# Performance work log

Measured on AMD Instinct MI355X. Metric: run time of the kernel, lower is better.

The kernel has to match this reference:

```python
import jax, jax.numpy as jnp
import numpy as np

EMBED_DIM = 1024
NUM_HEADS = 16
HEAD_DIM = EMBED_DIM // NUM_HEADS


def setup_inputs() -> dict:
    key = jax.random.key(0)
    k_x, k_wqkv, k_bqkv, k_wo, k_bo = jax.random.split(key, 5)
    B, T, C = 4, 2048, EMBED_DIM
    bound = 1.0 / np.sqrt(C)
    return {
        "x": jax.random.normal(k_x, (B, T, C), dtype=jnp.float32),
        "w_qkv": jax.random.uniform(k_wqkv, (C, 3 * C), jnp.float32, -bound, bound),
        "b_qkv": jax.random.uniform(k_bqkv, (3 * C,), jnp.float32, -bound, bound),
        "w_out": jax.random.uniform(k_wo, (C, C), jnp.float32, -bound, bound),
        "b_out": jax.random.uniform(k_bo, (C,), jnp.float32, -bound, bound),
    }


def reference(x, w_qkv, b_qkv, w_out, b_out):
    B, T, C = x.shape
    H, D = NUM_HEADS, HEAD_DIM
    qkv = x @ w_qkv + b_qkv                       # [B,T,3C]
    qkv = qkv.reshape(B, T, 3, H, D)
    q, k, v = qkv[:, :, 0], qkv[:, :, 1], qkv[:, :, 2]  # [B,T,H,D]
    scale = 1.0 / np.sqrt(D).astype(np.float32)
    scores = jnp.einsum("bqhd,bkhd->bhqk", q, k) * scale  # [B,H,T,T]
    causal = jnp.tril(jnp.ones((T, T), dtype=bool))
    scores = jnp.where(causal, scores, -jnp.inf)
    attn = jax.nn.softmax(scores, axis=-1)
    # dropout p=0.0 / eval mode -> identity
    ctx = jnp.einsum("bhqk,bkhd->bqhd", attn, v).reshape(B, T, C)
    return ctx @ w_out + b_out
```

## Files before the change

kernel.cpp:

```cpp
#include <hip/hip_runtime.h>
#include <hip/hip_bf16.h>

#define NB 4
#define NT 2048
#define NC 1024
#define NH 16
#define ND 64
#define BT (NB*NT)
#define LOG2E 1.4426950408889634f
#define NEG_BIG (-3.0e38f)
#define MLC 28.853900817779268f

typedef __attribute__((ext_vector_type(8))) short bf16x8;
typedef __attribute__((ext_vector_type(4))) float f32x4;

static __device__ __forceinline__ short f2bf(float f) {
    union { float f; unsigned u; } v; v.f = f;
    unsigned r = (v.u + 0x7fffu + ((v.u >> 16) & 1u)) >> 16;
    return (short)r;
}

static __device__ __forceinline__ unsigned pk2(float a, float b) {
#if __has_builtin(__builtin_amdgcn_cvt_pk_bf16_f32)
    auto v = __builtin_amdgcn_cvt_pk_bf16_f32(a, b);
    union { decltype(v) v; unsigned u; } c; c.v = v; return c.u;
#else
    return (unsigned)(unsigned short)f2bf(a) | ((unsigned)(unsigned short)f2bf(b) << 16);
#endif
}

static __device__ __forceinline__ f32x4 mfma16(bf16x8 a, bf16x8 b, f32x4 c) {
    return __builtin_amdgcn_mfma_f32_16x16x32_bf16(a, b, c, 0, 0, 0);
}

static __device__ __forceinline__ float fexp2(float x) {
#if __has_builtin(__builtin_amdgcn_exp2f)
    return __builtin_amdgcn_exp2f(x);
#else
    return exp2f(x);
#endif
}

template<int GOFF>
static __device__ __forceinline__ void gload_lds16(const short* g, short* l) {
    __builtin_amdgcn_global_load_lds(
        (const __attribute__((address_space(1))) void*)g,
        (__attribute__((address_space(3))) void*)l,
        16, GOFF, 0);
}

static __device__ __forceinline__ void wait_all() {
    __builtin_amdgcn_s_waitcnt(0);
    __builtin_amdgcn_sched_barrier(0);
}
static __device__ __forceinline__ void wait_lgkm() {
    __builtin_amdgcn_s_waitcnt(0xc07f);
    __builtin_amdgcn_sched_barrier(0);
}

__global__ __launch_bounds__(256)
void xcvt(const float* __restrict__ x, short* __restrict__ xb)
{
    const size_t i = ((size_t)blockIdx.x * 256 + threadIdx.x) * 8;
    float4 f0 = *(const float4*)(x + i);
    float4 f1 = *(const float4*)(x + i + 4);
    uint4 p;
    p.x = pk2(f0.x, f0.y); p.y = pk2(f0.z, f0.w);
    p.z = pk2(f1.x, f1.y); p.w = pk2(f1.z, f1.w);
    *(uint4*)(xb + i) = p;
}

__global__ __launch_bounds__(256)
void transpose_w(const float* __restrict__ w, short* __restrict__ wt, int R, int Cn)
{
    __shared__ short t[64][72];
    const int tid = threadIdx.x;
    const int r0 = blockIdx.x * 64;
    const int c0 = blockIdx.y * 64;
    {
        const int rl = tid >> 2, c4 = (tid & 3) << 4;
        const float* src = w + (size_t)(r0 + rl) * Cn + c0 + c4;
        float4 f0 = *(const float4*)(src + 0);
        float4 f1 = *(const float4*)(src + 4);
        float4 f2 = *(const float4*)(src + 8);
        float4 f3 = *(const float4*)(src + 12);
        short* d = &t[rl][c4];
        d[0]=f2bf(f0.x); d[1]=f2bf(f0.y); d[2]=f2bf(f0.z); d[3]=f2bf(f0.w);
        d[4]=f2bf(f1.x); d[5]=f2bf(f1.y); d[6]=f2bf(f1.z); d[7]=f2bf(f1.w);
        d[8]=f2bf(f2.x); d[9]=f2bf(f2.y); d[10]=f2bf(f2.z); d[11]=f2bf(f2.w);
        d[12]=f2bf(f3.x); d[13]=f2bf(f3.y); d[14]=f2bf(f3.z); d[15]=f2bf(f3.w);
    }
    __syncthreads();
    {
        const int cl = tid >> 2, r4 = (tid & 3) << 4;
        bf16x8 p0, p1;
#pragma unroll
        for (int j = 0; j < 8; ++j) { p0[j] = t[r4 + j][cl]; p1[j] = t[r4 + 8 + j][cl]; }
        short* dst = wt + (size_t)(c0 + cl) * R + r0 + r4;
        *(bf16x8*)dst       = p0;
        *(bf16x8*)(dst + 8) = p1;
    }
}

__global__ __launch_bounds__(256)
void qkv_gemm(const short* __restrict__ xb, const short* __restrict__ wt,
              const float* __restrict__ bias,
              short* __restrict__ q, short* __restrict__ k, short* __restrict__ vt)
{
    __shared__ short aLds[128 * 64];
    __shared__ short bLds[128 * 64];
    const int tid  = threadIdx.x;
    const int lane = tid & 63;
    const int wave = tid >> 6;
    const int waveM = wave & 1;
    const int waveN = wave >> 1;
    const int quad = lane >> 4;
    const int l15  = lane & 15;
    const int l7   = l15 & 7;
    const int m0 = blockIdx.x * 128;
    const int n0 = blockIdx.y * 128;

    const int rsub   = lane >> 3;
    const int cchunk = (lane & 7) ^ rsub;
    const int gcol   = cchunk * 8;

    f32x4 acc[4][4];
#pragma unroll
    for (int i = 0; i < 4; ++i)
#pragma unroll
        for (int j = 0; j < 4; ++j) acc[i][j] = 0.0f;

    for (int k0 = 0; k0 < NC; k0 += 64) {
#pragma unroll
        for (int i = 0; i < 4; ++i) {
            const int rbase = wave * 32 + i * 8;
            gload_lds16<0>(xb + (size_t)(m0 + rbase + rsub) * NC + k0 + gcol,
                           &aLds[rbase * 64]);
        }
#pragma unroll
        for (int i = 0; i < 4; ++i) {
            const int rbase = wave * 32 + i * 8;
            gload_lds16<0>(wt + (size_t)(n0 + rbase + rsub) * NC + k0 + gcol,
                           &bLds[rbase * 64]);
        }
        __syncthreads();

#pragma unroll
        for (int kd = 0; kd < 2; ++kd) {
            bf16x8 af[4], bfr[4];
#pragma unroll
            for (int mi = 0; mi < 4; ++mi) {
                const int r = waveM*64 + mi*16 + l15;
                af[mi] = *(const bf16x8*)&aLds[r*64 + (((kd*4 + quad) ^ l7) * 8)];
            }
#pragma unroll
            for (int ni = 0; ni < 4; ++ni) {
                const int r = waveN*64 + ni*16 + l15;
                bfr[ni] = *(const bf16x8*)&bLds[r*64 + (((kd*4 + quad) ^ l7) * 8)];
            }
#pragma unroll
            for (int mi = 0; mi < 4; ++mi)
#pragma unroll
                for (int ni = 0; ni < 4; ++ni)
                    acc[mi][ni] = mfma16(af[mi], bfr[ni], acc[mi][ni]);
        }
        __syncthreads();
    }

#pragma unroll
    for (int mi = 0; mi < 4; ++mi) {
#pragma unroll
        for (int ni = 0; ni < 4; ++ni) {
            const int n = n0 + waveN*64 + ni*16 + l15;
            const float bb = bias[n];
            const int s = n >> 10;
            const int h = (n >> 6) & 15;
            const int d = n & 63;
#pragma unroll
            for (int r = 0; r < 4; ++r) {
                const int m = m0 + waveM*64 + mi*16 + quad*4 + r;
                const int b = m >> 11;
                const int t = m & (NT - 1);
                const float val = acc[mi][ni][r] + bb;
                const size_t bhx = (size_t)(b * NH + h);
                if (s == 0)      q [(bhx * NT + t) * ND + d] = f2bf(val * 0.125f);
                else if (s == 1) k [(bhx * NT + t) * ND + d] = f2bf(val);
                else             vt[(bhx * ND + d) * NT + t] = f2bf(val);
            }
        }
    }
}

__global__ __launch_bounds__(64)
void attn(const short* __restrict__ q, const short* __restrict__ k,
          const short* __restrict__ vt, short* __restrict__ ctx)
{
    __shared__ short kbuf[64 * 64];
    __shared__ short vbuf[64 * 64];
    __shared__ short pLds[32][72];
    const int lane = threadIdx.x;
    const int quad = lane >> 4;
    const int l15  = lane & 15;
    const int l7   = l15 & 7;
    const int bh = blockIdx.x;
    const int b  = bh >> 4;
    const int h  = bh & 15;

    const short* Qp = q  + (size_t)bh * NT * ND;
    const short* Kp = k  + (size_t)bh * NT * ND;
    const short* Vp = vt + (size_t)bh * ND * NT;

    const int srow   = lane >> 3;
    const int schunk = ((lane & 7) ^ srow) * 8;

    for (int half = 0; half < 2; ++half) {
        const int qtile = half ? (63 - (int)blockIdx.y) : (int)blockIdx.y;
        const int wq0 = qtile * 32;
        const int ktend = (wq0 + 95) >> 6;

        bf16x8 qf[2][2];
#pragma unroll
        for (int mi = 0; mi < 2; ++mi)
#pragma unroll
            for (int kd = 0; kd < 2; ++kd)
                qf[mi][kd] = *(const bf16x8*)(Qp + (size_t)(wq0 + mi*16 + l15) * ND + kd*32 + quad*8);

        f32x4 ot[4][2];
        f32x4 lv[2];
#pragma unroll
        for (int di = 0; di < 4; ++di)
#pragma unroll
            for (int mi = 0; mi < 2; ++mi) ot[di][mi] = 0.0f;
        lv[0] = 0.0f; lv[1] = 0.0f;

        const short* Kcur = Kp + srow * ND + schunk;
        const short* Vg[8];
#pragma unroll
        for (int g = 0; g < 8; ++g)
            Vg[g] = Vp + (size_t)(g*8 + srow) * NT + schunk;

#pragma unroll
        for (int g = 0; g < 8; ++g)
            gload_lds16<0>(Kcur + g * 512, &kbuf[g * 512]);
#pragma unroll
        for (int g = 0; g < 8; ++g)
            gload_lds16<0>(Vg[g], &vbuf[g * 512]);

        for (int kt = 0; kt < ktend; ++kt) {
            wait_all();

            bf16x8 kf[4][2], vf[4][2];
#pragma unroll
            for (int ni = 0; ni < 4; ++ni)
#pragma unroll
                for (int kd = 0; kd < 2; ++kd)
                    kf[ni][kd] = *(const bf16x8*)
                        &kbuf[(ni*16 + l15)*64 + (((kd*4 + quad) ^ l7) * 8)];
#pragma unroll
            for (int di = 0; di < 4; ++di)
#pragma unroll
                for (int kd = 0; kd < 2; ++kd)
                    vf[di][kd] = *(const bf16x8*)
                        &vbuf[(di*16 + l15)*64 + (((kd*4 + quad) ^ l7) * 8)];
            wait_lgkm();

            if (kt + 1 < ktend) {
                Kcur += 4096;
#pragma unroll
                for (int g = 0; g < 8; ++g)
                    gload_lds16<0>(Kcur + g * 512, &kbuf[g * 512]);
#pragma unroll
                for (int g = 0; g < 8; ++g) {
                    Vg[g] += 64;
                    gload_lds16<0>(Vg[g], &vbuf[g * 512]);
                }
            }

            const int kb = kt << 6;

            f32x4 st[4][2];
#pragma unroll
            for (int ni = 0; ni < 4; ++ni)
#pragma unroll
                for (int mi = 0; mi < 2; ++mi) {
                    st[ni][mi] = 0.0f;
                    st[ni][mi] = mfma16(kf[ni][0], qf[mi][0], st[ni][mi]);
                    st[ni][mi] = mfma16(kf[ni][1], qf[mi][1], st[ni][mi]);
                }

            if (kb + 63 > wq0) {
#pragma unroll
                for (int ni = 0; ni < 4; ++ni)
#pragma unroll
                    for (int mi = 0; mi < 2; ++mi) {
                        const int qrow = wq0 + mi*16 + l15;
#pragma unroll
                        for (int r = 0; r < 4; ++r) {
                            const int key = kb + ni*16 + quad*4 + r;
                            if (key > qrow) st[ni][mi][r] = NEG_BIG;
                        }
                    }
            }

#pragma unroll
            for (int mi = 0; mi < 2; ++mi) {
#pragma unroll
                for (int ni = 0; ni < 4; ++ni) {
#pragma unroll
                    for (int r = 0; r < 4; ++r)
                        st[ni][mi][r] = fexp2(fmaf(st[ni][mi][r], LOG2E, -MLC));
                    lv[mi] += st[ni][mi];
                    const f32x4 v = st[ni][mi];
                    *(uint2*)&pLds[mi*16 + l15][ni*16 + quad*4] =
                        make_uint2(pk2(v[0], v[1]), pk2(v[2], v[3]));
                }
            }

            bf16x8 pf[2][2];
#pragma unroll
            for (int mi = 0; mi < 2; ++mi)
#pragma unroll
                for (int kd = 0; kd < 2; ++kd)
                    pf[mi][kd] = *(const bf16x8*)&pLds[mi*16 + l15][kd*32 + quad*8];

#pragma unroll
            for (int di = 0; di < 4; ++di)
#pragma unroll
                for (int mi = 0; mi < 2; ++mi) {
                    ot[di][mi] = mfma16(vf[di][0], pf[mi][0], ot[di][mi]);
                    ot[di][mi] = mfma16(vf[di][1], pf[mi][1], ot[di][mi]);
                }
        }

#pragma unroll
        for (int mi = 0; mi < 2; ++mi) {
            float l = lv[mi][0] + lv[mi][1] + lv[mi][2] + lv[mi][3];
            l += __shfl_xor(l, 16);
            l += __shfl_xor(l, 32);
            const float inv = 1.0f / l;
            const int t = wq0 + mi*16 + l15;
            short* dst = ctx + ((size_t)(b * NT + t)) * NC + h*64 + quad*4;
#pragma unroll
            for (int di = 0; di < 4; ++di) {
                const f32x4 v = ot[di][mi] * inv;
                *(uint2*)(dst + di*16) = make_uint2(pk2(v[0], v[1]), pk2(v[2], v[3]));
            }
        }
        wait_all();
    }
}

__global__ __launch_bounds__(256)
void out_gemm(const short* __restrict__ a, const short* __restrict__ wt,
              const float* __restrict__ bias, float* __restrict__ out)
{
    __shared__ short aLds[128 * 64];
    __shared__ short bLds[128 * 64];
    const int tid  = threadIdx.x;
    const int lane = tid & 63;
    const int wave = tid >> 6;
    const int waveM = wave & 1;
    const int waveN = wave >> 1;
    const int quad = lane >> 4;
    const int l15  = lane & 15;
    const int l7   = l15 & 7;
    const int m0 = blockIdx.x * 128;
    const int n0 = blockIdx.y * 128;

    const int rsub   = lane >> 3;
    const int cchunk = (lane & 7) ^ rsub;
    const int gcol   = cchunk * 8;

    f32x4 acc[4][4];
#pragma unroll
    for (int i = 0; i < 4; ++i)
#pragma unroll
        for (int j = 0; j < 4; ++j) acc[i][j] = 0.0f;

    for (int k0 = 0; k0 < NC; k0 += 64) {
#pragma unroll
        for (int i = 0; i < 4; ++i) {
            const int rbase = wave * 32 + i * 8;
            gload_lds16<0>(a + (size_t)(m0 + rbase + rsub) * NC + k0 + gcol,
                           &aLds[rbase * 64]);
        }
#pragma unroll
        for (int i = 0; i < 4; ++i) {
            const int rbase = wave * 32 + i * 8;
            gload_lds16<0>(wt + (size_t)(n0 + rbase + rsub) * NC + k0 + gcol,
                           &bLds[rbase * 64]);
        }
        __syncthreads();

#pragma unroll
        for (int kd = 0; kd < 2; ++kd) {
            bf16x8 af[4], bfr[4];
#pragma unroll
            for (int mi = 0; mi < 4; ++mi) {
                const int r = waveM*64 + mi*16 + l15;
                af[mi] = *(const bf16x8*)&aLds[r*64 + (((kd*4 + quad) ^ l7) * 8)];
            }
#pragma unroll
            for (int ni = 0; ni < 4; ++ni) {
                const int r = waveN*64 + ni*16 + l15;
                bfr[ni] = *(const bf16x8*)&bLds[r*64 + (((kd*4 + quad) ^ l7) * 8)];
            }
#pragma unroll
            for (int mi = 0; mi < 4; ++mi)
#pragma unroll
                for (int ni = 0; ni < 4; ++ni)
                    acc[mi][ni] = mfma16(af[mi], bfr[ni], acc[mi][ni]);
        }
        __syncthreads();
    }

#pragma unroll
    for (int mi = 0; mi < 4; ++mi) {
#pragma unroll
        for (int ni = 0; ni < 4; ++ni) {
            const int n = n0 + waveN*64 + ni*16 + l15;
            const float bb = bias[n];
#pragma unroll
            for (int r = 0; r < 4; ++r) {
                const int m = m0 + waveM*64 + mi*16 + quad*4 + r;
                out[(size_t)m * NC + n] = acc[mi][ni][r] + bb;
            }
        }
    }
}

extern "C" void kernel_launch(void* const* d_in, const int* in_sizes, int n_in,
                              void* d_out, int out_size, void* d_ws, size_t ws_size,
                              hipStream_t stream)
{
    const float* x     = (const float*)d_in[0];
    const float* w_qkv = (const float*)d_in[1];
    const float* b_qkv = (const float*)d_in[2];
    const float* w_out = (const float*)d_in[3];
    const float* b_out = (const float*)d_in[4];
    float* out = (float*)d_out;

    const size_t SZ = (size_t)NB * NH * NT * ND;
    short* q   = (short*)d_ws;
    short* kk  = q  + SZ;
    short* vt  = kk + SZ;
    short* ctx = vt + SZ;
    short* xbf = ctx + SZ;
    short* wTq = ctx;
    short* wTo = xbf;

    hipLaunchKernelGGL(xcvt, dim3(BT*NC/(256*8)), dim3(256), 0, stream, x, xbf);
    hipLaunchKernelGGL(transpose_w, dim3(16, 48), dim3(256), 0, stream,
                       w_qkv, wTq, NC, 3*NC);
    hipLaunchKernelGGL(qkv_gemm, dim3(BT/128, (3*NC)/128), dim3(256), 0, stream,
                       xbf, wTq, b_qkv, q, kk, vt);
    hipLaunchKernelGGL(attn, dim3(NB*NH, NT/64), dim3(64), 0, stream,
                       q, kk, vt, ctx);
    hipLaunchKernelGGL(transpose_w, dim3(16, 16), dim3(256), 0, stream,
                       w_out, wTo, NC, NC);
    hipLaunchKernelGGL(out_gemm, dim3(BT/128, NC/128), dim3(256), 0, stream,
                       ctx, wTo, b_out, out);
}
```

Measured before the change: 310.9 us.

## Share K/V tiles across four waves with double-buffered LDS in attention

The attention kernel moves from one wave per block to four waves, each handling 32 query rows of a 128-row block, so each K/V tile loaded into LDS is reused by four waves. K and V are double-buffered, with the next tile prefetched after a block barrier. The per-wave P scratch gets an XOR swizzle to avoid bank conflicts. This adds block-wide syncs each step, and waves past their causal limit sit idle at the barriers while still helping load.

```diff
diff --git a/kernel.cpp b/kernel.cpp
--- a/kernel.cpp
+++ b/kernel.cpp
@@ -47,15 +47,6 @@
         (const __attribute__((address_space(1))) void*)g,
         (__attribute__((address_space(3))) void*)l,
         16, GOFF, 0);
-}
-
-static __device__ __forceinline__ void wait_all() {
-    __builtin_amdgcn_s_waitcnt(0);
-    __builtin_amdgcn_sched_barrier(0);
-}
-static __device__ __forceinline__ void wait_lgkm() {
-    __builtin_amdgcn_s_waitcnt(0xc07f);
-    __builtin_amdgcn_sched_barrier(0);
 }
 
 __global__ __launch_bounds__(256)
@@ -191,14 +182,16 @@
     }
 }
 
-__global__ __launch_bounds__(64)
+__global__ __launch_bounds__(256)
 void attn(const short* __restrict__ q, const short* __restrict__ k,
           const short* __restrict__ vt, short* __restrict__ ctx)
 {
-    __shared__ short kbuf[64 * 64];
-    __shared__ short vbuf[64 * 64];
-    __shared__ short pLds[32][72];
-    const int lane = threadIdx.x;
+    __shared__ short kbuf[2][64 * 64];
+    __shared__ short vbuf[2][64 * 64];
+    __shared__ short pbuf[4][32 * 64];
+    const int tid  = threadIdx.x;
+    const int lane = tid & 63;
+    const int wave = tid >> 6;
     const int quad = lane >> 4;
     const int l15  = lane & 15;
     const int l7   = l15 & 7;
@@ -212,11 +205,13 @@
 
     const int srow   = lane >> 3;
     const int schunk = ((lane & 7) ^ srow) * 8;
+    short* pw = &pbuf[wave][0];
 
     for (int half = 0; half < 2; ++half) {
-        const int qtile = half ? (63 - (int)blockIdx.y) : (int)blockIdx.y;
-        const int wq0 = qtile * 32;
-        const int ktend = (wq0 + 95) >> 6;
+        const int qblock = half ? (15 - (int)blockIdx.y) : (int)blockIdx.y;
+        const int qb  = qblock * 128;
+        const int wq0 = qb + wave * 32;
+        const int ktB = 2 * qblock + 2;
 
         bf16x8 qf[2][2];
 #pragma unroll
@@ -233,50 +228,39 @@
             for (int mi = 0; mi < 2; ++mi) ot[di][mi] = 0.0f;
         lv[0] = 0.0f; lv[1] = 0.0f;
 
-        const short* Kcur = Kp + srow * ND + schunk;
-        const short* Vg[8];
-#pragma unroll
-        for (int g = 0; g < 8; ++g)
-            Vg[g] = Vp + (size_t)(g*8 + srow) * NT + schunk;
-
-#pragma unroll
-        for (int g = 0; g < 8; ++g)
-            gload_lds16<0>(Kcur + g * 512, &kbuf[g * 512]);
-#pragma unroll
-        for (int g = 0; g < 8; ++g)
-            gload_lds16<0>(Vg[g], &vbuf[g * 512]);
-
-        for (int kt = 0; kt < ktend; ++kt) {
-            wait_all();
-
-            bf16x8 kf[4][2], vf[4][2];
+        {
+            const short* Ks = Kp + (size_t)(wave*16 + srow) * ND + schunk;
+            gload_lds16<0>(Ks,          &kbuf[0][(wave*16    ) * 64]);
+            gload_lds16<0>(Ks + 8*ND,   &kbuf[0][(wave*16 + 8) * 64]);
+            const short* Vs = Vp + (size_t)(wave*16 + srow) * NT + schunk;
+            gload_lds16<0>(Vs,          &vbuf[0][(wave*16    ) * 64]);
+            gload_lds16<0>(Vs + 8*NT,   &vbuf[0][(wave*16 + 8) * 64]);
+        }
+
+        for (int kt = 0; kt < ktB; ++kt) {
+            const int p  = kt & 1;
+            const int kb = kt << 6;
+            __syncthreads();
+
+            if (kt + 1 < ktB) {
+                const int kb2 = kb + 64;
+                const short* Ks = Kp + (size_t)(kb2 + wave*16 + srow) * ND + schunk;
+                gload_lds16<0>(Ks,        &kbuf[1-p][(wave*16    ) * 64]);
+                gload_lds16<0>(Ks + 8*ND, &kbuf[1-p][(wave*16 + 8) * 64]);
+                const short* Vs = Vp + (size_t)(wave*16 + srow) * NT + kb2 + schunk;
+                gload_lds16<0>(Vs,        &vbuf[1-p][(wave*16    ) * 64]);
+                gload_lds16<0>(Vs + 8*NT, &vbuf[1-p][(wave*16 + 8) * 64]);
+            }
+
+            if (kb > wq0 + 31) continue;
+
+            bf16x8 kf[4][2];
 #pragma unroll
             for (int ni = 0; ni < 4; ++ni)
 #pragma unroll
                 for (int kd = 0; kd < 2; ++kd)
                     kf[ni][kd] = *(const bf16x8*)
-                        &kbuf[(ni*16 + l15)*64 + (((kd*4 + quad) ^ l7) * 8)];
-#pragma unroll
-            for (int di = 0; di < 4; ++di)
-#pragma unroll
-                for (int kd = 0; kd < 2; ++kd)
-                    vf[di][kd] = *(const bf16x8*)
-                        &vbuf[(di*16 + l15)*64 + (((kd*4 + quad) ^ l7) * 8)];
-            wait_lgkm();
-
-            if (kt + 1 < ktend) {
-                Kcur += 4096;
-#pragma unroll
-                for (int g = 0; g < 8; ++g)
-                    gload_lds16<0>(Kcur + g * 512, &kbuf[g * 512]);
-#pragma unroll
-                for (int g = 0; g < 8; ++g) {
-                    Vg[g] += 64;
-                    gload_lds16<0>(Vg[g], &vbuf[g * 512]);
-                }
-            }
-
-            const int kb = kt << 6;
+                        &kbuf[p][(ni*16 + l15)*64 + (((kd*4 + quad) ^ l7) * 8)];
 
             f32x4 st[4][2];
 #pragma unroll
@@ -311,17 +295,26 @@
                         st[ni][mi][r] = fexp2(fmaf(st[ni][mi][r], LOG2E, -MLC));
                     lv[mi] += st[ni][mi];
                     const f32x4 v = st[ni][mi];
-                    *(uint2*)&pLds[mi*16 + l15][ni*16 + quad*4] =
+                    *(uint2*)&pw[(mi*16 + l15)*64
+                                 + (((2*ni + (quad >> 1)) ^ l7) * 8)
+                                 + (quad & 1) * 4] =
                         make_uint2(pk2(v[0], v[1]), pk2(v[2], v[3]));
                 }
             }
 
-            bf16x8 pf[2][2];
+            bf16x8 vf[4][2], pf[2][2];
+#pragma unroll
+            for (int di = 0; di < 4; ++di)
+#pragma unroll
+                for (int kd = 0; kd < 2; ++kd)
+                    vf[di][kd] = *(const bf16x8*)
+                        &vbuf[p][(di*16 + l15)*64 + (((kd*4 + quad) ^ l7) * 8)];
 #pragma unroll
             for (int mi = 0; mi < 2; ++mi)
 #pragma unroll
                 for (int kd = 0; kd < 2; ++kd)
-                    pf[mi][kd] = *(const bf16x8*)&pLds[mi*16 + l15][kd*32 + quad*8];
+                    pf[mi][kd] = *(const bf16x8*)
+                        &pw[(mi*16 + l15)*64 + (((kd*4 + quad) ^ l7) * 8)];
 
 #pragma unroll
             for (int di = 0; di < 4; ++di)
@@ -346,7 +339,7 @@
                 *(uint2*)(dst + di*16) = make_uint2(pk2(v[0], v[1]), pk2(v[2], v[3]));
             }
         }
-        wait_all();
+        __syncthreads();
     }
 }
 
@@ -454,7 +447,7 @@
                        w_qkv, wTq, NC, 3*NC);
     hipLaunchKernelGGL(qkv_gemm, dim3(BT/128, (3*NC)/128), dim3(256), 0, stream,
                        xbf, wTq, b_qkv, q, kk, vt);
-    hipLaunchKernelGGL(attn, dim3(NB*NH, NT/64), dim3(64), 0, stream,
+    hipLaunchKernelGGL(attn, dim3(NB*NH, 8), dim3(256), 0, stream,
                        q, kk, vt, ctx);
     hipLaunchKernelGGL(transpose_w, dim3(16, 16), dim3(256), 0, stream,
                        w_out, wTo, NC, NC);
```

Result: faster. 276.2 us (-11.1%).
